# Optimization experiments

Hardware: AMD Instinct MI355X
Metric: run time of the kernel (lower is better)

## Reference

```python
import jax, jax.numpy as jnp
import numpy as np

V = 50000
E = 640000
DIM = 128
NUM_EDGE_TYPES = 32


def setup_inputs() -> dict:
    key = jax.random.key(0)
    ks = jax.random.split(key, 8)
    return {
        "node_values": jax.random.normal(ks[0], (V, DIM), dtype=jnp.float32),
        "edge_src": jax.random.randint(ks[1], (E,), 0, V, dtype=jnp.int32),
        "edge_dest": jax.random.randint(ks[2], (E,), 0, V, dtype=jnp.int32),
        "edge_cls": jax.random.randint(ks[3], (E,), 0, NUM_EDGE_TYPES, dtype=jnp.int32),
        "W_src": jax.random.normal(ks[4], (DIM, DIM), dtype=jnp.float32) / np.sqrt(DIM),
        "b_src": jnp.zeros((DIM,), dtype=jnp.float32),
        "W_dest": jax.random.normal(ks[5], (DIM, DIM), dtype=jnp.float32) / np.sqrt(DIM),
        "b_dest": jnp.zeros((DIM,), dtype=jnp.float32),
        "edge_emb": jax.random.normal(ks[6], (NUM_EDGE_TYPES, DIM), dtype=jnp.float32),
    }


def reference(node_values, edge_src, edge_dest, edge_cls, W_src, b_src, W_dest, b_dest, edge_emb):
    # Dense projections over all nodes, then gather per edge (matches tf.gather(dense(...), idx))
    src_proj = node_values @ W_src + b_src    # [V, dim]
    dest_proj = node_values @ W_dest + b_dest  # [V, dim]
    # Per-edge fused message: gather src, gather dest, edge-class embedding lookup, add, relu
    msgs = jax.nn.relu(src_proj[edge_src] + dest_proj[edge_dest] + edge_emb[edge_cls])  # [E, dim]
    # Scatter-reduce messages onto destination nodes
    out = jax.ops.segment_sum(msgs, edge_dest, num_segments=V)  # [V, dim]
    return out
```

## Files before the change

kernel.cpp:

```cpp
#include <hip/hip_runtime.h>


#define V 50000
#define E 640000
#define DIM 128
#define NXCD 8
#define NBIN_R 50
#define BINW 125
#define NBINS 400
#define BINCAP 2048
#define QCAP 384
#define NCHUNK 256
#define CSRN 2500
#define EC4 625
#define NPROJ 782
#define NFUSED 1038

typedef __bf16 bf16x8 __attribute__((ext_vector_type(8)));
typedef float  f32x4  __attribute__((ext_vector_type(4)));
typedef float  f32x2  __attribute__((ext_vector_type(2)));

__device__ __forceinline__ float bf2f(unsigned int u16) {
    union { unsigned int i; float f; } c; c.i = u16 << 16; return c.f;
}
__device__ __forceinline__ unsigned int f2bf(float f) {
    union { float f; unsigned int i; } c; c.f = f;
    unsigned int u = c.i;
    return (u + 0x7FFFu + ((u >> 16) & 1u)) >> 16;
}

__global__ __launch_bounds__(256) void mp_setup(
    const float* __restrict__ Ws, const float* __restrict__ Wd,
    const float* __restrict__ emb,
    unsigned short* __restrict__ Wpk, unsigned short* __restrict__ embB,
    int* __restrict__ binCnt)
{
    int tid = blockIdx.x * 256 + threadIdx.x;
    int mat  = tid >> 11;
    int rem  = tid & 2047;
    int ct   = rem >> 8;
    int kt   = (rem >> 6) & 3;
    int lane = rem & 63;
    const float* W = mat ? Wd : Ws;
    int n  = ct * 16 + (lane & 15);
    int k0 = kt * 32 + (lane >> 4) * 8;
    unsigned short* dst = Wpk + (size_t)tid * 8;
    #pragma unroll
    for (int j = 0; j < 8; ++j) dst[j] = (unsigned short)f2bf(W[(k0 + j) * DIM + n]);
    embB[tid] = (unsigned short)f2bf(emb[tid]);
    if (tid < NBINS) binCnt[tid] = 0;
}

__global__ __launch_bounds__(256) void mp_fused(
    const int* __restrict__ ed, const int* __restrict__ es, const int* __restrict__ ec,
    int* __restrict__ binCnt, int* __restrict__ binbuf,
    const float* __restrict__ x, const unsigned short* __restrict__ Wpk,
    const float* __restrict__ bs, const float* __restrict__ bd,
    unsigned char* __restrict__ ps8, unsigned short* __restrict__ pdB)
{
    __shared__ float stage[4][16 * 132];

    const int b = blockIdx.x;
    const int t = threadIdx.x;
    const bool isBin = ((b & 3) == 3) && (b < 1024);

    if (isBin) {
        int* base  = (int*)&stage[0][0];
        int* hist  = base;
        int* lofs  = base + 400;
        int* lcur  = base + 801;
        int* gbase = base + 1201;
        int* csr   = base + 1601;
        unsigned short* sbin = (unsigned short*)(base + 4101);

        const int c = b >> 2;

        for (int i = t; i < NBINS; i += 256) hist[i] = 0;

        int4 DV[3], SV[3], CV[3];
        {
            const int4* ed4 = (const int4*)ed + (size_t)c * EC4;
            const int4* es4 = (const int4*)es + (size_t)c * EC4;
            const int4* ec4 = (const int4*)ec + (size_t)c * EC4;
            #pragma unroll
            for (int k = 0; k < 3; ++k) {
                int i = t + k * 256;
                if (i < EC4) { DV[k] = ed4[i]; SV[k] = es4[i]; CV[k] = ec4[i]; }
                else { DV[k] = make_int4(-1, -1, -1, -1);
                       SV[k] = make_int4(0, 0, 0, 0); CV[k] = make_int4(0, 0, 0, 0); }
            }
        }
        __syncthreads();

        #pragma unroll
        for (int k = 0; k < 3; ++k) {
            #define H1(D) if ((D) >= 0) atomicAdd(&hist[(unsigned)(D) / BINW], 1);
            H1(DV[k].x); H1(DV[k].y); H1(DV[k].z); H1(DV[k].w);
            #undef H1
        }
        __syncthreads();

        for (int i = t; i < NBINS; i += 256)
            gbase[i] = atomicAdd(&binCnt[i], hist[i]);
        if (t < 64) {
            int carry = 0;
            #pragma unroll
            for (int s = 0; s < 7; ++s) {
                int idx = s * 64 + t;
                int v = (idx < NBINS) ? hist[idx] : 0;
                #pragma unroll
                for (int dlt = 1; dlt < 64; dlt <<= 1) {
                    int u = __shfl_up(v, dlt, 64);
                    if (t >= dlt) v += u;
                }
                int tot = __shfl(v, 63, 64);
                v += carry;
                if (idx < NBINS) { lofs[idx + 1] = v; lcur[idx] = v - hist[idx]; }
                carry += tot;
            }
            if (t == 0) lofs[0] = 0;
        }
        __syncthreads();

        #pragma unroll
        for (int k = 0; k < 3; ++k) {
            #define SC1(D, S, C) if ((D) >= 0) { \
                int bn = (unsigned)(D) / BINW; \
                int rl = (D) - bn * BINW; \
                int pos = atomicAdd(&lcur[bn], 1); \
                csr[pos] = ((S) & 0xFFFF) | ((C) << 16) | (rl << 21); \
                sbin[pos] = (unsigned short)bn; }
            SC1(DV[k].x, SV[k].x, CV[k].x); SC1(DV[k].y, SV[k].y, CV[k].y);
            SC1(DV[k].z, SV[k].z, CV[k].z); SC1(DV[k].w, SV[k].w, CV[k].w);
            #undef SC1
        }
        __syncthreads();

        for (int i = t; i < CSRN; i += 256) {
            int bb = sbin[i];
            int slot = gbase[bb] + (i - lofs[bb]);
            if (slot < BINCAP)
                binbuf[(size_t)bb * BINCAP + slot] = csr[i];
        }
        return;
    }

    const int p = (b < 1024) ? (b - ((b + 1) >> 2)) : (b - 256);
    if (p >= NPROJ) return;
    const int wave = __builtin_amdgcn_readfirstlane(threadIdx.x) >> 6;
    const int lane = threadIdx.x & 63;
    const int m = lane & 15, q = lane >> 4;
    const int row0 = p * 64 + wave * 16;

    int arow = row0 + m; if (arow >= V) arow = V - 1;
    const float* xr = x + (size_t)arow * DIM + q * 8;

    bf16x8 A[4];
    #pragma unroll
    for (int kt = 0; kt < 4; ++kt) {
        float4 u = *(const float4*)(xr + kt * 32);
        float4 v = *(const float4*)(xr + kt * 32 + 4);
        bf16x8 a;
        a[0] = (__bf16)u.x; a[1] = (__bf16)u.y; a[2] = (__bf16)u.z; a[3] = (__bf16)u.w;
        a[4] = (__bf16)v.x; a[5] = (__bf16)v.y; a[6] = (__bf16)v.z; a[7] = (__bf16)v.w;
        A[kt] = a;
    }

    const bf16x8* Bp = (const bf16x8*)Wpk;

    f32x4 accS[8], accD[8];
    #pragma unroll
    for (int ct = 0; ct < 8; ++ct) {
        f32x4 aS = {0.f, 0.f, 0.f, 0.f}, aD = {0.f, 0.f, 0.f, 0.f};
        #pragma unroll
        for (int kt = 0; kt < 4; ++kt) {
            bf16x8 bS = Bp[((0 * 8 + ct) * 4 + kt) * 64 + lane];
            bf16x8 bD = Bp[((1 * 8 + ct) * 4 + kt) * 64 + lane];
            aS = __builtin_amdgcn_mfma_f32_16x16x32_bf16(A[kt], bS, aS, 0, 0, 0);
            aD = __builtin_amdgcn_mfma_f32_16x16x32_bf16(A[kt], bD, aD, 0, 0, 0);
        }
        accS[ct] = aS; accD[ct] = aD;
    }

    float* st = stage[wave];
    const int rr = lane & 15, cg = lane >> 4;
    const int orow = row0 + rr;
    const float* rowp = st + rr * 132 + cg * 32;

    #pragma unroll
    for (int ct = 0; ct < 8; ++ct) {
        const float bv = bs[ct * 16 + m];
        #pragma unroll
        for (int rg = 0; rg < 4; ++rg)
            st[(q * 4 + rg) * 132 + ct * 16 + m] = accS[ct][rg] + bv;
    }
    __syncthreads();
    {
        int w[8];
        #pragma unroll
        for (int j = 0; j < 8; ++j) {
            float4 f = *(const float4*)(rowp + 4 * j);
            int v = __builtin_amdgcn_cvt_pk_fp8_f32(f.x, f.y, 0, false);
            v = __builtin_amdgcn_cvt_pk_fp8_f32(f.z, f.w, v, true);
            w[j] = v;
        }
        if (orow < V) {
            int4* dst = (int4*)(ps8 + (size_t)orow * 128 + cg * 32);
            dst[0] = make_int4(w[0], w[1], w[2], w[3]);
            dst[1] = make_int4(w[4], w[5], w[6], w[7]);
        }
    }
    __syncthreads();

    #pragma unroll
    for (int ct = 0; ct < 8; ++ct) {
        const float bv = bd[ct * 16 + m];
        #pragma unroll
        for (int rg = 0; rg < 4; ++rg)
            st[(q * 4 + rg) * 132 + ct * 16 + m] = accD[ct][rg] + bv;
    }
    __syncthreads();
    {
        int w[16];
        #pragma unroll
        for (int j = 0; j < 8; ++j) {
            float4 f = *(const float4*)(rowp + 4 * j);
            w[2 * j]     = f2bf(f.x) | (f2bf(f.y) << 16);
            w[2 * j + 1] = f2bf(f.z) | (f2bf(f.w) << 16);
        }
        if (orow < V) {
            int4* dst = (int4*)(pdB + (size_t)orow * 128 + cg * 32);
            #pragma unroll
            for (int jj = 0; jj < 4; ++jj)
                dst[jj] = make_int4(w[4 * jj], w[4 * jj + 1], w[4 * jj + 2], w[4 * jj + 3]);
        }
    }
}

__global__ __launch_bounds__(256) void mp_binBC(
    const unsigned char* __restrict__ ps8, const unsigned short* __restrict__ pdB,
    const unsigned short* __restrict__ embB,
    const int* __restrict__ binCnt, const int* __restrict__ binbuf,
    float* __restrict__ out)
{
    __shared__ int csr[QCAP];
    __shared__ int cnt[16];
    __shared__ int off[17];
    __shared__ int cur[16];

    const int r = blockIdx.x & (NXCD - 1);
    const int rest = blockIdx.x >> 3;
    const int bi = rest % NBIN_R;
    const int qu = rest / NBIN_R;
    const int bin = r * NBIN_R + bi;
    const int rel0 = qu * 16;
    const int relW = (qu == 7) ? 13 : 16;
    const int d0 = bin * BINW + rel0;
    const int t = threadIdx.x;
    const int wave = t >> 6, lane = t & 63;

    int nb = binCnt[bin]; if (nb > BINCAP) nb = BINCAP;
    const int* buf = binbuf + (size_t)bin * BINCAP;

    if (t < 16) cnt[t] = 0;

    int EB[8];
    #pragma unroll
    for (int k = 0; k < 8; ++k) {
        int i = t + k * 256;
        EB[k] = (i < nb) ? buf[i] : -1;
    }

    float dp0v[4], dp1v[4];
    #pragma unroll
    for (int k = 0; k < 4; ++k) {
        int rl = wave + k * 4;
        int d = d0 + ((rl < relW) ? rl : 0);
        unsigned int pdu = *(const unsigned int*)(pdB + (size_t)d * DIM + 2 * lane);
        dp0v[k] = bf2f(pdu & 0xFFFF); dp1v[k] = bf2f(pdu >> 16);
    }
    __syncthreads();

    #pragma unroll
    for (int k = 0; k < 8; ++k) {
        int rl = (int)((unsigned)EB[k] >> 21) - rel0;
        if ((unsigned)rl < (unsigned)relW) atomicAdd(&cnt[rl], 1);
    }
    __syncthreads();

    if (t < 16) {
        int v = (t < relW) ? cnt[t] : 0;
        #pragma unroll
        for (int dlt = 1; dlt < 16; dlt <<= 1) {
            int u = __shfl_up(v, dlt, 64);
            if (t >= dlt) v += u;
        }
        off[t + 1] = v;
        cur[t] = v - cnt[t];
        if (t == 0) off[0] = 0;
    }
    __syncthreads();

    #pragma unroll
    for (int k = 0; k < 8; ++k) {
        int rl = (int)((unsigned)EB[k] >> 21) - rel0;
        if ((unsigned)rl < (unsigned)relW) {
            int pos = atomicAdd(&cur[rl], 1);
            if (pos < QCAP) csr[pos] = EB[k];
        }
    }
    __syncthreads();

    #define PROC(P) { \
        int s_ = *(const unsigned short*)(ps8 + ((size_t)((P) & 0xFFFF) << 7) + 2 * lane); \
        unsigned int e_ = *(const unsigned int*)(embB + ((((P) >> 16) & 0x1F) << 7) + 2 * lane); \
        f32x2 f_ = __builtin_amdgcn_cvt_pk_f32_fp8(s_, false); \
        a0 += fmaxf(f_.x + dp0 + bf2f(e_ & 0xFFFF), 0.f); \
        a1 += fmaxf(f_.y + dp1 + bf2f(e_ >> 16),    0.f); }

    #pragma unroll
    for (int k = 0; k < 4; ++k) {
        const int rl = wave + k * 4;
        if (rl >= relW) break;
        const int d = d0 + rl;
        int i0 = off[rl], i1 = off[rl + 1];
        if (i1 > QCAP) i1 = QCAP;
        if (i0 > i1) i0 = i1;
        const float dp0 = dp0v[k], dp1 = dp1v[k];
        float a0 = 0.f, a1 = 0.f;
        int i = i0;
        for (; i + 8 <= i1; i += 8) {
            int p0 = csr[i],     p1 = csr[i + 1], p2 = csr[i + 2], p3 = csr[i + 3];
            int p4 = csr[i + 4], p5 = csr[i + 5], p6 = csr[i + 6], p7 = csr[i + 7];
            PROC(p0); PROC(p1); PROC(p2); PROC(p3);
            PROC(p4); PROC(p5); PROC(p6); PROC(p7);
        }
        for (; i + 4 <= i1; i += 4) {
            int p0 = csr[i], p1 = csr[i + 1], p2 = csr[i + 2], p3 = csr[i + 3];
            PROC(p0); PROC(p1); PROC(p2); PROC(p3);
        }
        for (; i < i1; ++i) { int p0 = csr[i]; PROC(p0); }
        *(float2*)(out + (size_t)d * DIM + 2 * lane) = make_float2(a0, a1);
    }
    #undef PROC
}

extern "C" void kernel_launch(void* const* d_in, const int* in_sizes, int n_in,
                              void* d_out, int out_size, void* d_ws, size_t ws_size,
                              hipStream_t stream) {
    const float* x   = (const float*)d_in[0];
    const int*   es  = (const int*)d_in[1];
    const int*   ed  = (const int*)d_in[2];
    const int*   ec  = (const int*)d_in[3];
    const float* Ws  = (const float*)d_in[4];
    const float* bs  = (const float*)d_in[5];
    const float* Wd  = (const float*)d_in[6];
    const float* bd  = (const float*)d_in[7];
    const float* emb = (const float*)d_in[8];
    float* out = (float*)d_out;

    char* ws = (char*)d_ws;
    size_t off = 0;
    unsigned char*  ps8  = (unsigned char*)(ws + off);  off += (size_t)V * 128;
    unsigned short* pdB  = (unsigned short*)(ws + off); off += (size_t)V * DIM * 2;
    int* binbuf = (int*)(ws + off);                     off += (size_t)NBINS * BINCAP * 4;
    int* binCnt = (int*)(ws + off);                     off += (size_t)NBINS * 4;
    unsigned short* Wpk  = (unsigned short*)(ws + off); off += 2 * 128 * 128 * 2;
    unsigned short* embB = (unsigned short*)(ws + off); off += 32 * 128 * 2;

    mp_setup<<<16, 256, 0, stream>>>(Ws, Wd, emb, Wpk, embB, binCnt);
    mp_fused<<<NFUSED, 256, 0, stream>>>(ed, es, ec, binCnt, binbuf,
                                         x, Wpk, bs, bd, ps8, pdB);
    mp_binBC<<<NBIN_R * NXCD * 8, 256, 0, stream>>>(ps8, pdB, embB, binCnt, binbuf, out);
}
```

Measured before the change: 147.5 us.

## Split src/dest MFMA phases, prefetch B tiles, pad LDS, stage embeddings in LDS

The projection kernel now computes the src and dest accumulators in separate phases instead of holding both sets of accumulators live. This cuts register pressure, and the kernel requests 4 blocks per CU through launch bounds. Each phase double-buffers its weight fragment loads, and the LDS staging row stride is padded from 132 to 133 to change bank mapping. The scatter kernel copies the bf16 edge embedding table into shared memory so per-edge embedding reads hit LDS instead of global memory, at the cost of 8KB extra LDS and a copy per block.

```diff
diff --git a/kernel.cpp b/kernel.cpp
--- a/kernel.cpp
+++ b/kernel.cpp
@@ -15,6 +15,7 @@
 #define EC4 625
 #define NPROJ 782
 #define NFUSED 1038
+#define SPAD 133
 
 typedef __bf16 bf16x8 __attribute__((ext_vector_type(8)));
 typedef float  f32x4  __attribute__((ext_vector_type(4)));
@@ -51,14 +52,14 @@
     if (tid < NBINS) binCnt[tid] = 0;
 }
 
-__global__ __launch_bounds__(256) void mp_fused(
+__global__ __launch_bounds__(256, 4) void mp_fused(
     const int* __restrict__ ed, const int* __restrict__ es, const int* __restrict__ ec,
     int* __restrict__ binCnt, int* __restrict__ binbuf,
     const float* __restrict__ x, const unsigned short* __restrict__ Wpk,
     const float* __restrict__ bs, const float* __restrict__ bd,
     unsigned char* __restrict__ ps8, unsigned short* __restrict__ pdB)
 {
-    __shared__ float stage[4][16 * 132];
+    __shared__ float stage[4][16 * SPAD];
 
     const int b = blockIdx.x;
     const int t = threadIdx.x;
@@ -168,31 +169,38 @@
 
     const bf16x8* Bp = (const bf16x8*)Wpk;
 
-    f32x4 accS[8], accD[8];
-    #pragma unroll
-    for (int ct = 0; ct < 8; ++ct) {
-        f32x4 aS = {0.f, 0.f, 0.f, 0.f}, aD = {0.f, 0.f, 0.f, 0.f};
-        #pragma unroll
-        for (int kt = 0; kt < 4; ++kt) {
-            bf16x8 bS = Bp[((0 * 8 + ct) * 4 + kt) * 64 + lane];
-            bf16x8 bD = Bp[((1 * 8 + ct) * 4 + kt) * 64 + lane];
-            aS = __builtin_amdgcn_mfma_f32_16x16x32_bf16(A[kt], bS, aS, 0, 0, 0);
-            aD = __builtin_amdgcn_mfma_f32_16x16x32_bf16(A[kt], bD, aD, 0, 0, 0);
-        }
-        accS[ct] = aS; accD[ct] = aD;
-    }
-
     float* st = stage[wave];
     const int rr = lane & 15, cg = lane >> 4;
     const int orow = row0 + rr;
-    const float* rowp = st + rr * 132 + cg * 32;
-
-    #pragma unroll
-    for (int ct = 0; ct < 8; ++ct) {
-        const float bv = bs[ct * 16 + m];
-        #pragma unroll
-        for (int rg = 0; rg < 4; ++rg)
-            st[(q * 4 + rg) * 132 + ct * 16 + m] = accS[ct][rg] + bv;
+    const float* rowp = st + rr * SPAD + cg * 32;
+
+    {
+        f32x4 acc[8];
+        bf16x8 b0[4], b1[4];
+        #pragma unroll
+        for (int kt = 0; kt < 4; ++kt) b0[kt] = Bp[(0 * 32 + 0 * 4 + kt) * 64 + lane];
+        #pragma unroll
+        for (int ct = 0; ct < 8; ++ct) {
+            if (ct < 7) {
+                #pragma unroll
+                for (int kt = 0; kt < 4; ++kt)
+                    b1[kt] = Bp[(0 * 32 + (ct + 1) * 4 + kt) * 64 + lane];
+            }
+            f32x4 a = {0.f, 0.f, 0.f, 0.f};
+            #pragma unroll
+            for (int kt = 0; kt < 4; ++kt)
+                a = __builtin_amdgcn_mfma_f32_16x16x32_bf16(A[kt], b0[kt], a, 0, 0, 0);
+            acc[ct] = a;
+            #pragma unroll
+            for (int kt = 0; kt < 4; ++kt) b0[kt] = b1[kt];
+        }
+        #pragma unroll
+        for (int ct = 0; ct < 8; ++ct) {
+            const float bv = bs[ct * 16 + m];
+            #pragma unroll
+            for (int rg = 0; rg < 4; ++rg)
+                st[(q * 4 + rg) * SPAD + ct * 16 + m] = acc[ct][rg] + bv;
+        }
     }
     __syncthreads();
     {
@@ -212,12 +220,33 @@
     }
     __syncthreads();
 
-    #pragma unroll
-    for (int ct = 0; ct < 8; ++ct) {
-        const float bv = bd[ct * 16 + m];
-        #pragma unroll
-        for (int rg = 0; rg < 4; ++rg)
-            st[(q * 4 + rg) * 132 + ct * 16 + m] = accD[ct][rg] + bv;
+    {
+        f32x4 acc[8];
+        bf16x8 b0[4], b1[4];
+        #pragma unroll
+        for (int kt = 0; kt < 4; ++kt) b0[kt] = Bp[(1 * 32 + 0 * 4 + kt) * 64 + lane];
+        #pragma unroll
+        for (int ct = 0; ct < 8; ++ct) {
+            if (ct < 7) {
+                #pragma unroll
+                for (int kt = 0; kt < 4; ++kt)
+                    b1[kt] = Bp[(1 * 32 + (ct + 1) * 4 + kt) * 64 + lane];
+            }
+            f32x4 a = {0.f, 0.f, 0.f, 0.f};
+            #pragma unroll
+            for (int kt = 0; kt < 4; ++kt)
+                a = __builtin_amdgcn_mfma_f32_16x16x32_bf16(A[kt], b0[kt], a, 0, 0, 0);
+            acc[ct] = a;
+            #pragma unroll
+            for (int kt = 0; kt < 4; ++kt) b0[kt] = b1[kt];
+        }
+        #pragma unroll
+        for (int ct = 0; ct < 8; ++ct) {
+            const float bv = bd[ct * 16 + m];
+            #pragma unroll
+            for (int rg = 0; rg < 4; ++rg)
+                st[(q * 4 + rg) * SPAD + ct * 16 + m] = acc[ct][rg] + bv;
+        }
     }
     __syncthreads();
     {
@@ -247,6 +276,7 @@
     __shared__ int cnt[16];
     __shared__ int off[17];
     __shared__ int cur[16];
+    __shared__ unsigned short sEmb[32 * DIM];
 
     const int r = blockIdx.x & (NXCD - 1);
     const int rest = blockIdx.x >> 3;
@@ -264,6 +294,13 @@
 
     if (t < 16) cnt[t] = 0;
 
+    {
+        const int4* s4 = (const int4*)embB;
+        int4* d4 = (int4*)sEmb;
+        d4[t] = s4[t];
+        d4[t + 256] = s4[t + 256];
+    }
+
     int EB[8];
     #pragma unroll
     for (int k = 0; k < 8; ++k) {
@@ -313,7 +350,7 @@
 
     #define PROC(P) { \
         int s_ = *(const unsigned short*)(ps8 + ((size_t)((P) & 0xFFFF) << 7) + 2 * lane); \
-        unsigned int e_ = *(const unsigned int*)(embB + ((((P) >> 16) & 0x1F) << 7) + 2 * lane); \
+        unsigned int e_ = *(const unsigned int*)(sEmb + ((((P) >> 16) & 0x1F) << 7) + 2 * lane); \
         f32x2 f_ = __builtin_amdgcn_cvt_pk_f32_fp8(s_, false); \
         a0 += fmaxf(f_.x + dp0 + bf2f(e_ & 0xFFFF), 0.f); \
         a1 += fmaxf(f_.y + dp1 + bf2f(e_ >> 16),    0.f); }
```

After: 136.5 us. -7.4%, faster.
